# Performance work log

Hardware: AMD Instinct MI355X
Metric: run time of the kernel (lower is better)

## Reference

```python
import jax, jax.numpy as jnp
import numpy as np

B, L, INP, HID = 32, 1024, 600, 200

def setup_inputs() -> dict:
    key = jax.random.key(0)
    k1, k2, k3, k4 = jax.random.split(key, 4)
    return {
        "s1": jax.random.normal(k1, (B, L, INP), dtype=jnp.float32),
        "s2": jax.random.normal(k2, (B, L, INP), dtype=jnp.float32),
        "mask1": jnp.ones((B, L), dtype=jnp.float32),
        "mask2": jnp.ones((B, L), dtype=jnp.float32),
        "W1": jax.random.normal(k3, (INP, HID), dtype=jnp.float32) * (1.0 / np.sqrt(INP)),
        "b1": jnp.zeros((HID,), dtype=jnp.float32),
        "W2": jax.random.normal(k4, (HID, HID), dtype=jnp.float32) * (1.0 / np.sqrt(HID)),
        "b2": jnp.zeros((HID,), dtype=jnp.float32),
    }

def _mlp(x, W1, b1, W2, b2):
    # Dropout is identity at inference; two Linear+ReLU layers.
    h = jax.nn.relu(x @ W1 + b1)
    return jax.nn.relu(h @ W2 + b2)

def reference(s1, s2, mask1, mask2, W1, b1, W2, b2):
    h1 = _mlp(s1, W1, b1, W2, b2)          # (b, L, hid)
    h2 = _mlp(s2, W1, b1, W2, b2)          # (b, L, hid)
    e = jnp.einsum('bld,bmd->blm', h1, h2) # (b, LA, LB)
    # alpha: mask rows by mask1, softmax over LA (axis=1)
    e_alpha = jax.nn.softmax(e * mask1[:, :, None], axis=1)
    # beta: mask cols by mask2, softmax over LB (axis=2)
    e_beta = jax.nn.softmax(e * mask2[:, None, :], axis=2)
    alphas = jnp.einsum('blm,bld->bmd', e_alpha, s1) * mask2[:, :, None]
    betas = jnp.einsum('blm,bmd->bld', e_beta, s2) * mask1[:, :, None]
    return alphas, betas
```

## Files before the change

### kernel.cpp

```cpp
#include <hip/hip_runtime.h>
#include <math.h>

namespace {

constexpr int BB  = 32;
constexpr int LL  = 1024;
constexpr int INP = 600;
constexpr int HID = 200;
constexpr int RS  = BB * LL;
constexpr int DPAD = 640;

constexpr int BM = 128, BN = 128, KT = 8;

typedef __attribute__((ext_vector_type(8))) short short8v;
typedef __attribute__((ext_vector_type(8))) unsigned short ushort8v;
typedef __attribute__((ext_vector_type(4))) float f32x4;

__device__ __forceinline__ float relu(float x) { return fmaxf(x, 0.f); }

__device__ __forceinline__ unsigned short f2bf(float x) {
  union { float f; unsigned int u; } v; v.f = x;
  unsigned int r = v.u + 0x7FFFu + ((v.u >> 16) & 1u);
  return (unsigned short)(r >> 16);
}
__device__ __forceinline__ float bf2f(unsigned short h) {
  union { unsigned int u; float f; } v; v.u = ((unsigned int)h) << 16;
  return v.f;
}

__device__ __forceinline__ void gload16(const void* g, void* l) {
  __builtin_amdgcn_global_load_lds((const __attribute__((address_space(1))) void*)g,
                                   (__attribute__((address_space(3))) void*)l, 16, 0, 0);
}

__global__ __launch_bounds__(256) void wt_prep(
    const float* __restrict__ W, unsigned short* __restrict__ Whi, unsigned short* __restrict__ Wlo,
    int K, int KP)
{
  const int k = blockIdx.x * 256 + threadIdx.x;
  const int n = blockIdx.y;
  if (k >= KP) return;
  float v = (k < K && n < HID) ? W[(size_t)k * HID + n] : 0.f;
  unsigned short hi = f2bf(v);
  unsigned short lo = f2bf(v - bf2f(hi));
  Whi[(size_t)n * KP + k] = hi;
  Wlo[(size_t)n * KP + k] = lo;
}

template <bool MLP>
__global__ __launch_bounds__(256) void splitmm(
    const float* __restrict__ A0, const float* __restrict__ A1, long aZ, int lda, int ka,
    const float* __restrict__ Bf, long bZ,
    const unsigned short* __restrict__ Bhi, const unsigned short* __restrict__ Blo,
    int ldb, int kb, int ksteps,
    const float* __restrict__ bias,
    float* __restrict__ Out, int ldo, long oZ)
{
  __shared__ int4 sA[2048];
  __shared__ int4 sB[2048];
  const int z = blockIdx.z;
  const int m0 = blockIdx.x * 128, n0 = blockIdx.y * 128;
  const int tid = threadIdx.x, lane = tid & 63, w = tid >> 6;
  const int wr = w >> 1, wc = w & 1, fr = lane & 15, kg = lane >> 4;

  const float* __restrict__ A = MLP ? (z ? A1 : A0) : (A0 + (size_t)z * aZ);
  const float* __restrict__ Bp = MLP ? (const float*)nullptr : (Bf + (size_t)z * bZ);

  const int ar = tid >> 1, aseg = tid & 1;

  f32x4 acc[4][4];
#pragma unroll
  for (int mi = 0; mi < 4; ++mi)
#pragma unroll
    for (int ni = 0; ni < 4; ++ni) acc[mi][ni] = (f32x4){0.f, 0.f, 0.f, 0.f};

  for (int ks = 0; ks < ksteps; ++ks) {
    const int k0 = ks * 64;
    __syncthreads();
#pragma unroll
    for (int u = 0; u < 4; ++u) {
      const int c = aseg * 4 + u;
      const int gk = k0 + c * 8;
      float4 v0 = make_float4(0.f, 0.f, 0.f, 0.f), v1 = v0;
      if (gk < ka) {
        const float* p = A + (size_t)(m0 + ar) * lda + gk;
        v0 = *(const float4*)p;
        v1 = *(const float4*)(p + 4);
      }
      ushort8v hv, lv;
      hv[0] = f2bf(v0.x); lv[0] = f2bf(v0.x - bf2f(hv[0]));
      hv[1] = f2bf(v0.y); lv[1] = f2bf(v0.y - bf2f(hv[1]));
      hv[2] = f2bf(v0.z); lv[2] = f2bf(v0.z - bf2f(hv[2]));
      hv[3] = f2bf(v0.w); lv[3] = f2bf(v0.w - bf2f(hv[3]));
      hv[4] = f2bf(v1.x); lv[4] = f2bf(v1.x - bf2f(hv[4]));
      hv[5] = f2bf(v1.y); lv[5] = f2bf(v1.y - bf2f(hv[5]));
      hv[6] = f2bf(v1.z); lv[6] = f2bf(v1.z - bf2f(hv[6]));
      hv[7] = f2bf(v1.w); lv[7] = f2bf(v1.w - bf2f(hv[7]));
      const int slot = ar * 8 + (c ^ (ar & 7));
      *(ushort8v*)&sA[slot] = hv;
      *(ushort8v*)&sA[1024 + slot] = lv;
    }
    if (MLP) {
#pragma unroll
      for (int i = 0; i < 8; ++i) {
        const int s = w * 512 + i * 64 + lane;
        const int tens = s >> 10, rem = s & 1023, r = rem >> 3, kc = rem & 7;
        const int gc = kc ^ (r & 7);
        const unsigned short* src = (tens ? Blo : Bhi) + (size_t)(n0 + r) * ldb + k0 + gc * 8;
        gload16(src, (char*)sB + ((size_t)(w * 512 + i * 64)) * 16);
      }
    } else {
#pragma unroll
      for (int u = 0; u < 4; ++u) {
        const int c = aseg * 4 + u;
        const int gk = k0 + c * 8;
        float4 v0 = make_float4(0.f, 0.f, 0.f, 0.f), v1 = v0;
        if (gk < kb) {
          const float* p = Bp + (size_t)(n0 + ar) * ldb + gk;
          v0 = *(const float4*)p;
          v1 = *(const float4*)(p + 4);
        }
        ushort8v hv, lv;
        hv[0] = f2bf(v0.x); lv[0] = f2bf(v0.x - bf2f(hv[0]));
        hv[1] = f2bf(v0.y); lv[1] = f2bf(v0.y - bf2f(hv[1]));
        hv[2] = f2bf(v0.z); lv[2] = f2bf(v0.z - bf2f(hv[2]));
        hv[3] = f2bf(v0.w); lv[3] = f2bf(v0.w - bf2f(hv[3]));
        hv[4] = f2bf(v1.x); lv[4] = f2bf(v1.x - bf2f(hv[4]));
        hv[5] = f2bf(v1.y); lv[5] = f2bf(v1.y - bf2f(hv[5]));
        hv[6] = f2bf(v1.z); lv[6] = f2bf(v1.z - bf2f(hv[6]));
        hv[7] = f2bf(v1.w); lv[7] = f2bf(v1.w - bf2f(hv[7]));
        const int slot = ar * 8 + (c ^ (ar & 7));
        *(ushort8v*)&sB[slot] = hv;
        *(ushort8v*)&sB[1024 + slot] = lv;
      }
    }
    __syncthreads();
#pragma unroll
    for (int kk = 0; kk < 2; ++kk) {
      short8v ah[4], al[4], bh[4], bl[4];
#pragma unroll
      for (int mi = 0; mi < 4; ++mi) {
        const int row = wr * 64 + mi * 16 + fr;
        const int idx = row * 8 + ((kk * 4 + kg) ^ (row & 7));
        ah[mi] = *(const short8v*)&sA[idx];
        al[mi] = *(const short8v*)&sA[1024 + idx];
      }
#pragma unroll
      for (int ni = 0; ni < 4; ++ni) {
        const int row = wc * 64 + ni * 16 + fr;
        const int idx = row * 8 + ((kk * 4 + kg) ^ (row & 7));
        bh[ni] = *(const short8v*)&sB[idx];
        bl[ni] = *(const short8v*)&sB[1024 + idx];
      }
#pragma unroll
      for (int mi = 0; mi < 4; ++mi)
#pragma unroll
        for (int ni = 0; ni < 4; ++ni) {
          acc[mi][ni] = __builtin_amdgcn_mfma_f32_16x16x32_bf16(ah[mi], bh[ni], acc[mi][ni], 0, 0, 0);
          acc[mi][ni] = __builtin_amdgcn_mfma_f32_16x16x32_bf16(ah[mi], bl[ni], acc[mi][ni], 0, 0, 0);
          acc[mi][ni] = __builtin_amdgcn_mfma_f32_16x16x32_bf16(al[mi], bh[ni], acc[mi][ni], 0, 0, 0);
        }
    }
  }
#pragma unroll
  for (int ni = 0; ni < 4; ++ni) {
    const int gn = n0 + wc * 64 + ni * 16 + fr;
    if (!MLP || gn < HID) {
      const float bs = MLP ? bias[gn] : 0.f;
#pragma unroll
      for (int mi = 0; mi < 4; ++mi) {
#pragma unroll
        for (int r = 0; r < 4; ++r) {
          const int gm = m0 + wr * 64 + mi * 16 + kg * 4 + r;
          float v = acc[mi][ni][r] + bs;
          if (MLP) v = relu(v);
          Out[(size_t)z * oZ + (size_t)gm * ldo + gn] = v;
        }
      }
    }
  }
}

__global__ __launch_bounds__(256) void row_stats_pbeta(
    const float* __restrict__ E, const float* __restrict__ mask2,
    unsigned short* __restrict__ Pb)
{
  const int wid = threadIdx.x >> 6, lane = threadIdx.x & 63;
  const int r = blockIdx.x * 4 + wid;
  const int b = r >> 10;
  const float* __restrict__ row = E + (size_t)r * LL;
  const float* __restrict__ m2 = mask2 + b * LL;
  float v[16];
  float mx = -INFINITY;
#pragma unroll
  for (int i = 0; i < 4; ++i) {
    const int m = lane * 4 + i * 256;
    float4 e4 = *(const float4*)(row + m);
    float4 k4 = *(const float4*)(m2 + m);
    v[i * 4 + 0] = e4.x * k4.x; v[i * 4 + 1] = e4.y * k4.y;
    v[i * 4 + 2] = e4.z * k4.z; v[i * 4 + 3] = e4.w * k4.w;
    mx = fmaxf(mx, fmaxf(fmaxf(v[i * 4], v[i * 4 + 1]), fmaxf(v[i * 4 + 2], v[i * 4 + 3])));
  }
#pragma unroll
  for (int off = 32; off; off >>= 1) mx = fmaxf(mx, __shfl_xor(mx, off));
  float s = 0.f;
#pragma unroll
  for (int i = 0; i < 16; ++i) s += __expf(v[i] - mx);
#pragma unroll
  for (int off = 32; off; off >>= 1) s += __shfl_xor(s, off);
  const float ri = 1.f / s;
#pragma unroll
  for (int i = 0; i < 4; ++i) {
    const int m = lane * 4 + i * 256;
    ushort4 o;
    o.x = f2bf(__expf(v[i * 4 + 0] - mx) * ri);
    o.y = f2bf(__expf(v[i * 4 + 1] - mx) * ri);
    o.z = f2bf(__expf(v[i * 4 + 2] - mx) * ri);
    o.w = f2bf(__expf(v[i * 4 + 3] - mx) * ri);
    *(ushort4*)(Pb + (size_t)r * LL + m) = o;
  }
}

__global__ __launch_bounds__(256) void col_stats_p1(
    const float* __restrict__ E, const float* __restrict__ mask1,
    float* __restrict__ pmax, float* __restrict__ psum)
{
  const int b = blockIdx.z, lc = blockIdx.y;
  const int m = blockIdx.x * 256 + threadIdx.x;
  const float* __restrict__ e = E + (size_t)b * LL * LL;
  const float* __restrict__ m1 = mask1 + b * LL;
  float mx = -INFINITY, s = 0.f;
#pragma unroll 4
  for (int l = lc * 256; l < lc * 256 + 256; ++l) {
    const float v = e[(size_t)l * LL + m] * m1[l];
    if (v > mx) { s = s * __expf(mx - v) + 1.f; mx = v; }
    else        { s += __expf(v - mx); }
  }
  const int idx = (b * 4 + lc) * LL + m;
  pmax[idx] = mx; psum[idx] = s;
}

__global__ __launch_bounds__(256) void col_stats_p2(
    const float* __restrict__ pmax, const float* __restrict__ psum,
    float* __restrict__ cmax, float* __restrict__ cinv)
{
  const int b = blockIdx.y;
  const int m = blockIdx.x * 256 + threadIdx.x;
  float M = -INFINITY;
#pragma unroll
  for (int i = 0; i < 4; ++i) M = fmaxf(M, pmax[(b * 4 + i) * LL + m]);
  float S = 0.f;
#pragma unroll
  for (int i = 0; i < 4; ++i) S += psum[(b * 4 + i) * LL + m] * __expf(pmax[(b * 4 + i) * LL + m] - M);
  cmax[(size_t)b * LL + m] = M;
  cinv[(size_t)b * LL + m] = 1.f / S;
}

__global__ __launch_bounds__(256) void palpha_kernel(
    const float* __restrict__ E, const float* __restrict__ mask1,
    const float* __restrict__ cmax, const float* __restrict__ cinv,
    unsigned short* __restrict__ Pa)
{
  __shared__ float T[64][65];
  const int b = blockIdx.z;
  const int l0 = blockIdx.y * 64, m0 = blockIdx.x * 64;
  const int tid = threadIdx.x;
  const int rr = tid >> 4, c4 = (tid & 15) * 4;
  const float4 cm = *(const float4*)(cmax + b * LL + m0 + c4);
  const float4 ci = *(const float4*)(cinv + b * LL + m0 + c4);
#pragma unroll
  for (int it = 0; it < 4; ++it) {
    const int lloc = rr + it * 16;
    const int l = l0 + lloc;
    const float mk = mask1[b * LL + l];
    const float4 ev = *(const float4*)(E + ((size_t)b * LL + l) * LL + m0 + c4);
    T[c4 + 0][lloc] = __expf(ev.x * mk - cm.x) * ci.x;
    T[c4 + 1][lloc] = __expf(ev.y * mk - cm.y) * ci.y;
    T[c4 + 2][lloc] = __expf(ev.z * mk - cm.z) * ci.z;
    T[c4 + 3][lloc] = __expf(ev.w * mk - cm.w) * ci.w;
  }
  __syncthreads();
#pragma unroll
  for (int it = 0; it < 4; ++it) {
    const int mloc = rr + it * 16;
    ushort4 o;
    o.x = f2bf(T[mloc][c4 + 0]);
    o.y = f2bf(T[mloc][c4 + 1]);
    o.z = f2bf(T[mloc][c4 + 2]);
    o.w = f2bf(T[mloc][c4 + 3]);
    *(ushort4*)(Pa + ((size_t)b * LL + m0 + mloc) * LL + l0 + c4) = o;
  }
}

__global__ __launch_bounds__(256) void s_transpose(
    const float* __restrict__ S, unsigned short* __restrict__ St)
{
  __shared__ float T[64][65];
  const int b = blockIdx.z;
  const int l0 = blockIdx.y * 64, d0 = blockIdx.x * 64;
  const int tid = threadIdx.x;
  const int rr = tid >> 4, c4 = (tid & 15) * 4;
#pragma unroll
  for (int it = 0; it < 4; ++it) {
    const int lloc = rr + it * 16;
    const int l = l0 + lloc;
    float4 v = make_float4(0.f, 0.f, 0.f, 0.f);
    if (d0 + c4 < INP) v = *(const float4*)(S + ((size_t)b * LL + l) * INP + d0 + c4);
    T[c4 + 0][lloc] = v.x; T[c4 + 1][lloc] = v.y;
    T[c4 + 2][lloc] = v.z; T[c4 + 3][lloc] = v.w;
  }
  __syncthreads();
#pragma unroll
  for (int it = 0; it < 4; ++it) {
    const int dloc = rr + it * 16;
    ushort4 o;
    o.x = f2bf(T[dloc][c4 + 0]);
    o.y = f2bf(T[dloc][c4 + 1]);
    o.z = f2bf(T[dloc][c4 + 2]);
    o.w = f2bf(T[dloc][c4 + 3]);
    *(ushort4*)(St + ((size_t)b * DPAD + d0 + dloc) * LL + l0 + c4) = o;
  }
}

__global__ __launch_bounds__(256) void attn_gemm_bf16(
    const unsigned short* __restrict__ Ap, const unsigned short* __restrict__ Bt,
    const float* __restrict__ scale, float* __restrict__ Out)
{
  __shared__ int4 sAB[2048];
  __shared__ float s_sc[128];
  const int b  = blockIdx.z;
  const int n0 = blockIdx.x * 128;
  const int m0 = blockIdx.y * 128;
  const int tid = threadIdx.x;
  const int lane = tid & 63;
  const int w = tid >> 6;
  const int wr = w >> 1, wc = w & 1;
  const int fr = lane & 15, kg = lane >> 4;

  const unsigned short* __restrict__ A  = Ap + (size_t)b * LL * LL;
  const unsigned short* __restrict__ Bp = Bt + (size_t)b * DPAD * LL;

  if (tid < 128) s_sc[tid] = scale[b * LL + m0 + tid];

  f32x4 acc[4][4];
#pragma unroll
  for (int mi = 0; mi < 4; ++mi)
#pragma unroll
    for (int ni = 0; ni < 4; ++ni)
      acc[mi][ni] = (f32x4){0.f, 0.f, 0.f, 0.f};

  for (int k0 = 0; k0 < LL; k0 += 64) {
    __syncthreads();
#pragma unroll
    for (int i = 0; i < 8; ++i) {
      const int s = w * 512 + i * 64 + lane;
      const int tens = s >> 10, rem = s & 1023, r = rem >> 3, kc = rem & 7;
      const int gc = kc ^ (r & 7);
      const unsigned short* src = tens ? (Bp + (size_t)(n0 + r) * LL + k0 + gc * 8)
                                       : (A  + (size_t)(m0 + r) * LL + k0 + gc * 8);
      gload16(src, (char*)sAB + ((size_t)(w * 512 + i * 64)) * 16);
    }
    __syncthreads();
#pragma unroll
    for (int kk = 0; kk < 2; ++kk) {
      short8v a[4], bf[4];
#pragma unroll
      for (int mi = 0; mi < 4; ++mi) {
        const int row = wr * 64 + mi * 16 + fr;
        a[mi] = *(const short8v*)&sAB[row * 8 + ((kk * 4 + kg) ^ (row & 7))];
      }
#pragma unroll
      for (int ni = 0; ni < 4; ++ni) {
        const int row = wc * 64 + ni * 16 + fr;
        bf[ni] = *(const short8v*)&sAB[1024 + row * 8 + ((kk * 4 + kg) ^ (row & 7))];
      }
#pragma unroll
      for (int mi = 0; mi < 4; ++mi)
#pragma unroll
        for (int ni = 0; ni < 4; ++ni)
          acc[mi][ni] = __builtin_amdgcn_mfma_f32_16x16x32_bf16(a[mi], bf[ni], acc[mi][ni], 0, 0, 0);
    }
  }

#pragma unroll
  for (int mi = 0; mi < 4; ++mi) {
#pragma unroll
    for (int ni = 0; ni < 4; ++ni) {
      const int col = n0 + wc * 64 + ni * 16 + fr;
      if (col < INP) {
#pragma unroll
        for (int r = 0; r < 4; ++r) {
          const int mrow = wr * 64 + mi * 16 + kg * 4 + r;
          Out[((size_t)b * LL + m0 + mrow) * INP + col] = acc[mi][ni][r] * s_sc[mrow];
        }
      }
    }
  }
}

__device__ __forceinline__ void micro_8x8(const float (&sA)[KT][BM], const float (&sB)[KT][BN],
                                          float (&acc)[8][8], int tx, int ty)
{
#pragma unroll
  for (int kk = 0; kk < KT; ++kk) {
    float4 a0 = *(const float4*)&sA[kk][ty * 8];
    float4 a1 = *(const float4*)&sA[kk][ty * 8 + 4];
    float4 b0 = *(const float4*)&sB[kk][tx * 8];
    float4 b1 = *(const float4*)&sB[kk][tx * 8 + 4];
    float ar[8] = {a0.x, a0.y, a0.z, a0.w, a1.x, a1.y, a1.z, a1.w};
    float br[8] = {b0.x, b0.y, b0.z, b0.w, b1.x, b1.y, b1.z, b1.w};
#pragma unroll
    for (int i = 0; i < 8; ++i)
#pragma unroll
      for (int j = 0; j < 8; ++j)
        acc[i][j] = fmaf(ar[i], br[j], acc[i][j]);
  }
}

__global__ __launch_bounds__(256) void mlp_gemm(
    const float* __restrict__ A0, const float* __restrict__ A1,
    const float* __restrict__ W,  const float* __restrict__ bias,
    float* __restrict__ Out, int K)
{
  __shared__ __align__(16) float sA[KT][BM];
  __shared__ __align__(16) float sB[KT][BN];
  const int z = blockIdx.z;
  const float* __restrict__ A = z ? A1 : A0;
  float* __restrict__ out = Out + (size_t)z * RS * HID;
  const int m0 = blockIdx.x * BM;
  const int n0 = blockIdx.y * BN;
  const int tid = threadIdx.x;
  const int tx = tid & 15, ty = tid >> 4;
  const int am = tid & 127, akg = (tid >> 7) * 4;
  const int bn = (tid & 31) * 4, bkk = tid >> 5;

  float acc[8][8] = {};
  for (int k0 = 0; k0 < K; k0 += KT) {
    float4 av = *(const float4*)(A + (size_t)(m0 + am) * K + k0 + akg);
    sA[akg + 0][am] = av.x; sA[akg + 1][am] = av.y;
    sA[akg + 2][am] = av.z; sA[akg + 3][am] = av.w;
    const int gn = n0 + bn;
    float4 bv = make_float4(0.f, 0.f, 0.f, 0.f);
    if (gn < HID) bv = *(const float4*)(W + (size_t)(k0 + bkk) * HID + gn);
    *(float4*)&sB[bkk][bn] = bv;
    __syncthreads();
    micro_8x8(sA, sB, acc, tx, ty);
    __syncthreads();
  }
#pragma unroll
  for (int i = 0; i < 8; ++i) {
    const int m = m0 + ty * 8 + i;
#pragma unroll
    for (int j4 = 0; j4 < 8; j4 += 4) {
      const int n = n0 + tx * 8 + j4;
      if (n < HID) {
        float4 v;
        v.x = relu(acc[i][j4 + 0] + bias[n + 0]);
        v.y = relu(acc[i][j4 + 1] + bias[n + 1]);
        v.z = relu(acc[i][j4 + 2] + bias[n + 2]);
        v.w = relu(acc[i][j4 + 3] + bias[n + 3]);
        *(float4*)(out + (size_t)m * HID + n) = v;
      }
    }
  }
}

__global__ __launch_bounds__(256) void e_gemm(
    const float* __restrict__ H1, const float* __restrict__ H2, float* __restrict__ E)
{
  __shared__ __align__(16) float sA[KT][BM];
  __shared__ __align__(16) float sB[KT][BN];
  const int b = blockIdx.z;
  const float* __restrict__ A  = H1 + (size_t)b * LL * HID;
  const float* __restrict__ Bp = H2 + (size_t)b * LL * HID;
  float* __restrict__ e = E + (size_t)b * LL * LL;
  const int l0 = blockIdx.x * BM;
  const int m0 = blockIdx.y * BN;
  const int tid = threadIdx.x;
  const int tx = tid & 15, ty = tid >> 4;
  const int rr = tid & 127, kg = (tid >> 7) * 4;

  float acc[8][8] = {};
  for (int k0 = 0; k0 < HID; k0 += KT) {
    float4 av = *(const float4*)(A + (size_t)(l0 + rr) * HID + k0 + kg);
    sA[kg + 0][rr] = av.x; sA[kg + 1][rr] = av.y;
    sA[kg + 2][rr] = av.z; sA[kg + 3][rr] = av.w;
    float4 bv = *(const float4*)(Bp + (size_t)(m0 + rr) * HID + k0 + kg);
    sB[kg + 0][rr] = bv.x; sB[kg + 1][rr] = bv.y;
    sB[kg + 2][rr] = bv.z; sB[kg + 3][rr] = bv.w;
    __syncthreads();
    micro_8x8(sA, sB, acc, tx, ty);
    __syncthreads();
  }
#pragma unroll
  for (int i = 0; i < 8; ++i) {
    float* erow = e + (size_t)(l0 + ty * 8 + i) * LL + m0 + tx * 8;
    *(float4*)(erow)     = make_float4(acc[i][0], acc[i][1], acc[i][2], acc[i][3]);
    *(float4*)(erow + 4) = make_float4(acc[i][4], acc[i][5], acc[i][6], acc[i][7]);
  }
}

__global__ __launch_bounds__(256) void row_stats(
    const float* __restrict__ E, const float* __restrict__ mask2,
    float* __restrict__ rmax, float* __restrict__ rinv)
{
  const int wid = threadIdx.x >> 6, lane = threadIdx.x & 63;
  const int r = blockIdx.x * 4 + wid;
  const int b = r >> 10;
  const float* __restrict__ row = E + (size_t)r * LL;
  const float* __restrict__ m2 = mask2 + b * LL;
  float v[16];
  float mx = -INFINITY;
#pragma unroll
  for (int i = 0; i < 4; ++i) {
    const int m = lane * 4 + i * 256;
    float4 e4 = *(const float4*)(row + m);
    float4 k4 = *(const float4*)(m2 + m);
    v[i * 4 + 0] = e4.x * k4.x; v[i * 4 + 1] = e4.y * k4.y;
    v[i * 4 + 2] = e4.z * k4.z; v[i * 4 + 3] = e4.w * k4.w;
    mx = fmaxf(mx, fmaxf(fmaxf(v[i * 4], v[i * 4 + 1]), fmaxf(v[i * 4 + 2], v[i * 4 + 3])));
  }
#pragma unroll
  for (int off = 32; off; off >>= 1) mx = fmaxf(mx, __shfl_xor(mx, off));
  float s = 0.f;
#pragma unroll
  for (int i = 0; i < 16; ++i) s += __expf(v[i] - mx);
#pragma unroll
  for (int off = 32; off; off >>= 1) s += __shfl_xor(s, off);
  if (lane == 0) { rmax[r] = mx; rinv[r] = 1.f / s; }
}

__global__ __launch_bounds__(256) void alphas_gemm(
    const float* __restrict__ E, const float* __restrict__ S1,
    const float* __restrict__ mask1, const float* __restrict__ mask2,
    const float* __restrict__ cmax, const float* __restrict__ cinv,
    float* __restrict__ OutA)
{
  __shared__ __align__(16) float sA[KT][BM];
  __shared__ __align__(16) float sB[KT][BN];
  __shared__ __align__(16) float s_cm[BM], s_ci[BM], s_m2[BM];
  const int b = blockIdx.z;
  const float* __restrict__ e  = E  + (size_t)b * LL * LL;
  const float* __restrict__ s1 = S1 + (size_t)b * LL * INP;
  const int m0 = blockIdx.x * BM;
  const int d0 = blockIdx.y * BN;
  const int tid = threadIdx.x;
  const int tx = tid & 15, ty = tid >> 4;
  if (tid < BM) {
    s_cm[tid] = cmax[b * LL + m0 + tid];
    s_ci[tid] = cinv[b * LL + m0 + tid];
    s_m2[tid] = mask2[b * LL + m0 + tid];
  }
  __syncthreads();
  const int cc = (tid & 31) * 4, kk_ = tid >> 5;

  float acc[8][8] = {};
  for (int k0 = 0; k0 < LL; k0 += KT) {
    const int l = k0 + kk_;
    const float mk = mask1[b * LL + l];
    float4 ev = *(const float4*)(e + (size_t)l * LL + m0 + cc);
    float4 av;
    av.x = __expf(ev.x * mk - s_cm[cc + 0]) * s_ci[cc + 0];
    av.y = __expf(ev.y * mk - s_cm[cc + 1]) * s_ci[cc + 1];
    av.z = __expf(ev.z * mk - s_cm[cc + 2]) * s_ci[cc + 2];
    av.w = __expf(ev.w * mk - s_cm[cc + 3]) * s_ci[cc + 3];
    *(float4*)&sA[kk_][cc] = av;
    const int gd = d0 + cc;
    float4 bv = make_float4(0.f, 0.f, 0.f, 0.f);
    if (gd < INP) bv = *(const float4*)(s1 + (size_t)l * INP + gd);
    *(float4*)&sB[kk_][cc] = bv;
    __syncthreads();
    micro_8x8(sA, sB, acc, tx, ty);
    __syncthreads();
  }
#pragma unroll
  for (int i = 0; i < 8; ++i) {
    const int m = m0 + ty * 8 + i;
    const float mm = s_m2[ty * 8 + i];
    float* orow = OutA + ((size_t)b * LL + m) * INP;
#pragma unroll
    for (int j4 = 0; j4 < 8; j4 += 4) {
      const int d = d0 + tx * 8 + j4;
      if (d < INP) {
        *(float4*)(orow + d) = make_float4(acc[i][j4] * mm, acc[i][j4 + 1] * mm,
                                           acc[i][j4 + 2] * mm, acc[i][j4 + 3] * mm);
      }
    }
  }
}

__global__ __launch_bounds__(256) void betas_gemm(
    const float* __restrict__ E, const float* __restrict__ S2,
    const float* __restrict__ mask1, const float* __restrict__ mask2,
    const float* __restrict__ rmax, const float* __restrict__ rinv,
    float* __restrict__ OutB)
{
  __shared__ __align__(16) float sA[KT][BM];
  __shared__ __align__(16) float sB[KT][BN];
  __shared__ __align__(16) float s_rm[BM], s_ri[BM], s_m1[BM];
  const int b = blockIdx.z;
  const float* __restrict__ e  = E  + (size_t)b * LL * LL;
  const float* __restrict__ s2 = S2 + (size_t)b * LL * INP;
  const int l0 = blockIdx.x * BM;
  const int d0 = blockIdx.y * BN;
  const int tid = threadIdx.x;
  const int tx = tid & 15, ty = tid >> 4;
  if (tid < BM) {
    s_rm[tid] = rmax[b * LL + l0 + tid];
    s_ri[tid] = rinv[b * LL + l0 + tid];
    s_m1[tid] = mask1[b * LL + l0 + tid];
  }
  __syncthreads();
  const int al = tid & 127, akg = (tid >> 7) * 4;
  const int cc = (tid & 31) * 4, kk_ = tid >> 5;

  float acc[8][8] = {};
  for (int k0 = 0; k0 < LL; k0 += KT) {
    float4 ev = *(const float4*)(e + (size_t)(l0 + al) * LL + k0 + akg);
    float4 mk = *(const float4*)(mask2 + b * LL + k0 + akg);
    const float rm = s_rm[al], ri = s_ri[al];
    sA[akg + 0][al] = __expf(ev.x * mk.x - rm) * ri;
    sA[akg + 1][al] = __expf(ev.y * mk.y - rm) * ri;
    sA[akg + 2][al] = __expf(ev.z * mk.z - rm) * ri;
    sA[akg + 3][al] = __expf(ev.w * mk.w - rm) * ri;
    const int gd = d0 + cc;
    float4 bv = make_float4(0.f, 0.f, 0.f, 0.f);
    if (gd < INP) bv = *(const float4*)(s2 + (size_t)(k0 + kk_) * INP + gd);
    *(float4*)&sB[kk_][cc] = bv;
    __syncthreads();
    micro_8x8(sA, sB, acc, tx, ty);
    __syncthreads();
  }
#pragma unroll
  for (int i = 0; i < 8; ++i) {
    const int l = l0 + ty * 8 + i;
    const float mm = s_m1[ty * 8 + i];
    float* orow = OutB + ((size_t)b * LL + l) * INP;
#pragma unroll
    for (int j4 = 0; j4 < 8; j4 += 4) {
      const int d = d0 + tx * 8 + j4;
      if (d < INP) {
        *(float4*)(orow + d) = make_float4(acc[i][j4] * mm, acc[i][j4 + 1] * mm,
                                           acc[i][j4 + 2] * mm, acc[i][j4 + 3] * mm);
      }
    }
  }
}

}

extern "C" void kernel_launch(void* const* d_in, const int* in_sizes, int n_in,
                              void* d_out, int out_size, void* d_ws, size_t ws_size,
                              hipStream_t stream)
{
  const float* s1    = (const float*)d_in[0];
  const float* s2    = (const float*)d_in[1];
  const float* mask1 = (const float*)d_in[2];
  const float* mask2 = (const float*)d_in[3];
  const float* W1    = (const float*)d_in[4];
  const float* b1    = (const float*)d_in[5];
  const float* W2    = (const float*)d_in[6];
  const float* b2    = (const float*)d_in[7];

  char* ws = (char*)d_ws;
  float* outA = (float*)d_out;
  float* outB = outA + (size_t)BB * LL * INP;

  const size_t off_h  = 52428800;
  const size_t off_E  = 104857600;
  const size_t off_Pb = 239075328;
  const size_t TOTAL  = 306184192;

  if (ws_size >= TOTAL) {
    float* hmid = (float*)(ws + 0);
    float* h    = (float*)(ws + off_h);
    float* E    = (float*)(ws + off_E);
    unsigned short* Wt1hi = (unsigned short*)(ws + off_E);
    unsigned short* Wt1lo = Wt1hi + (size_t)256 * 640;
    unsigned short* Wt2hi = Wt1lo + (size_t)256 * 640;
    unsigned short* Wt2lo = Wt2hi + (size_t)256 * 256;
    unsigned short* Pb = (unsigned short*)(ws + off_Pb);
    unsigned short* Pa = (unsigned short*)(ws + 0);
    float* stats = (float*)(ws + 67108864);
    float* cmax = stats;
    float* cinv = cmax + RS;
    float* pmax = cinv + RS;
    float* psum = pmax + (size_t)BB * 4 * LL;
    unsigned short* s1t = (unsigned short*)(ws + off_E);
    unsigned short* s2t = s1t + (size_t)BB * DPAD * LL;

    wt_prep<<<dim3(3, 256), 256, 0, stream>>>(W1, Wt1hi, Wt1lo, INP, 640);
    wt_prep<<<dim3(1, 256), 256, 0, stream>>>(W2, Wt2hi, Wt2lo, HID, 256);
    splitmm<true><<<dim3(RS / 128, 2, 2), 256, 0, stream>>>(
        s1, s2, 0, INP, INP, nullptr, 0, Wt1hi, Wt1lo, 640, 0, 10,
        b1, hmid, HID, (long)RS * HID);
    splitmm<true><<<dim3(RS / 128, 2, 2), 256, 0, stream>>>(
        hmid, hmid + (size_t)RS * HID, 0, HID, HID, nullptr, 0, Wt2hi, Wt2lo, 256, 0, 4,
        b2, h, HID, (long)RS * HID);
    splitmm<false><<<dim3(8, 8, BB), 256, 0, stream>>>(
        h, nullptr, (long)LL * HID, HID, HID,
        h + (size_t)RS * HID, (long)LL * HID, nullptr, nullptr, HID, HID, 4,
        nullptr, E, LL, (long)LL * LL);
    row_stats_pbeta<<<dim3(RS / 4), 256, 0, stream>>>(E, mask2, Pb);
    col_stats_p1<<<dim3(4, 4, BB), 256, 0, stream>>>(E, mask1, pmax, psum);
    col_stats_p2<<<dim3(4, BB), 256, 0, stream>>>(pmax, psum, cmax, cinv);
    palpha_kernel<<<dim3(16, 16, BB), 256, 0, stream>>>(E, mask1, cmax, cinv, Pa);
    s_transpose<<<dim3(10, 16, BB), 256, 0, stream>>>(s1, s1t);
    s_transpose<<<dim3(10, 16, BB), 256, 0, stream>>>(s2, s2t);
    attn_gemm_bf16<<<dim3(5, 8, BB), 256, 0, stream>>>(Pb, s2t, mask1, outB);
    attn_gemm_bf16<<<dim3(5, 8, BB), 256, 0, stream>>>(Pa, s1t, mask2, outA);
  } else {
    float* h    = (float*)ws;
    float* hmid = h + (size_t)2 * RS * HID;
    float* E    = hmid;
    float* stats = hmid + (size_t)BB * LL * LL;
    float* rmax = stats;
    float* rinv = rmax + RS;
    float* cmax = rinv + RS;
    float* cinv = cmax + RS;
    float* pmax = cinv + RS;
    float* psum = pmax + (size_t)BB * 4 * LL;

    mlp_gemm<<<dim3(RS / BM, 2, 2), 256, 0, stream>>>(s1, s2, W1, b1, hmid, INP);
    mlp_gemm<<<dim3(RS / BM, 2, 2), 256, 0, stream>>>(hmid, hmid + (size_t)RS * HID, W2, b2, h, HID);
    e_gemm<<<dim3(LL / BM, LL / BN, BB), 256, 0, stream>>>(h, h + (size_t)RS * HID, E);
    row_stats<<<dim3(RS / 4), 256, 0, stream>>>(E, mask2, rmax, rinv);
    col_stats_p1<<<dim3(4, 4, BB), 256, 0, stream>>>(E, mask1, pmax, psum);
    col_stats_p2<<<dim3(4, BB), 256, 0, stream>>>(pmax, psum, cmax, cinv);
    alphas_gemm<<<dim3(LL / BM, (INP + BN - 1) / BN, BB), 256, 0, stream>>>(
        E, s1, mask1, mask2, cmax, cinv, outA);
    betas_gemm<<<dim3(LL / BM, (INP + BN - 1) / BN, BB), 256, 0, stream>>>(
        E, s2, mask1, mask2, rmax, rinv, outB);
  }

  (void)in_sizes; (void)n_in; (void)out_size;
}
```

Baseline: 926.4 us.

## Pre-split inputs to bf16 hi/lo and load all GEMM operands via LDS DMA

Adds a presplit kernel that converts s1/s2 into padded bf16 hi/lo arrays once, and makes the MLP GEMMs emit bf16 hi/lo split outputs directly. The unified splitmm2 kernel then loads both A and B operands with global_load_lds DMA instead of fp32 loads plus in-register conversion. This removes repeated fp32-to-bf16 splitting for every N tile and the VGPR and ALU pressure in the load path. In exchange it adds an extra pass over the inputs, writes split intermediates (the same total bytes as fp32), and reworks the workspace layout.

Result: no change. 927.7 us (+0.1%).

```diff
diff --git a/kernel.cpp b/kernel.cpp
--- a/kernel.cpp
+++ b/kernel.cpp
@@ -9,11 +9,12 @@
 constexpr int HID = 200;
 constexpr int RS  = BB * LL;
 constexpr int DPAD = 640;
+constexpr int KP1 = 640;
+constexpr int KP2 = 256;
 
 constexpr int BM = 128, BN = 128, KT = 8;
 
 typedef __attribute__((ext_vector_type(8))) short short8v;
-typedef __attribute__((ext_vector_type(8))) unsigned short ushort8v;
 typedef __attribute__((ext_vector_type(4))) float f32x4;
 
 __device__ __forceinline__ float relu(float x) { return fmaxf(x, 0.f); }
@@ -31,6 +32,26 @@
 __device__ __forceinline__ void gload16(const void* g, void* l) {
   __builtin_amdgcn_global_load_lds((const __attribute__((address_space(1))) void*)g,
                                    (__attribute__((address_space(3))) void*)l, 16, 0, 0);
+}
+
+__global__ __launch_bounds__(256) void presplit(
+    const float* __restrict__ S1, const float* __restrict__ S2,
+    unsigned short* __restrict__ Hi, unsigned short* __restrict__ Lo)
+{
+  const long idx = (long)blockIdx.x * 256 + threadIdx.x;
+  const long row = idx / 160;
+  const int  c4  = (int)(idx - row * 160) * 4;
+  const float* __restrict__ src = (row < RS) ? (S1 + row * (size_t)INP)
+                                             : (S2 + (row - RS) * (size_t)INP);
+  float4 v = make_float4(0.f, 0.f, 0.f, 0.f);
+  if (c4 < INP) v = *(const float4*)(src + c4);
+  ushort4 h4, l4;
+  h4.x = f2bf(v.x); l4.x = f2bf(v.x - bf2f(h4.x));
+  h4.y = f2bf(v.y); l4.y = f2bf(v.y - bf2f(h4.y));
+  h4.z = f2bf(v.z); l4.z = f2bf(v.z - bf2f(h4.z));
+  h4.w = f2bf(v.w); l4.w = f2bf(v.w - bf2f(h4.w));
+  *(ushort4*)(Hi + row * (size_t)KP1 + c4) = h4;
+  *(ushort4*)(Lo + row * (size_t)KP1 + c4) = l4;
 }
 
 __global__ __launch_bounds__(256) void wt_prep(
@@ -47,26 +68,29 @@
   Wlo[(size_t)n * KP + k] = lo;
 }
 
-template <bool MLP>
-__global__ __launch_bounds__(256) void splitmm(
-    const float* __restrict__ A0, const float* __restrict__ A1, long aZ, int lda, int ka,
-    const float* __restrict__ Bf, long bZ,
+template <bool SPLIT_OUT>
+__global__ __launch_bounds__(256) void splitmm2(
+    const unsigned short* __restrict__ Ahi, const unsigned short* __restrict__ Alo,
+    long aZ, int lda,
     const unsigned short* __restrict__ Bhi, const unsigned short* __restrict__ Blo,
-    int ldb, int kb, int ksteps,
-    const float* __restrict__ bias,
-    float* __restrict__ Out, int ldo, long oZ)
-{
-  __shared__ int4 sA[2048];
-  __shared__ int4 sB[2048];
+    long bZ, int ldb,
+    int ksteps, const float* __restrict__ bias,
+    unsigned short* __restrict__ OutHi, unsigned short* __restrict__ OutLo,
+    float* __restrict__ OutF, int ldo, long oZ)
+{
+  __shared__ int4 sL[4096];
   const int z = blockIdx.z;
   const int m0 = blockIdx.x * 128, n0 = blockIdx.y * 128;
   const int tid = threadIdx.x, lane = tid & 63, w = tid >> 6;
   const int wr = w >> 1, wc = w & 1, fr = lane & 15, kg = lane >> 4;
 
-  const float* __restrict__ A = MLP ? (z ? A1 : A0) : (A0 + (size_t)z * aZ);
-  const float* __restrict__ Bp = MLP ? (const float*)nullptr : (Bf + (size_t)z * bZ);
-
-  const int ar = tid >> 1, aseg = tid & 1;
+  const unsigned short* __restrict__ wbase =
+      (w == 0) ? (Ahi + (size_t)z * aZ) :
+      (w == 1) ? (Alo + (size_t)z * aZ) :
+      (w == 2) ? (Bhi + (size_t)z * bZ) :
+                 (Blo + (size_t)z * bZ);
+  const int wrow0 = (w < 2) ? m0 : n0;
+  const int wld   = (w < 2) ? lda : ldb;
 
   f32x4 acc[4][4];
 #pragma unroll
@@ -78,61 +102,12 @@
     const int k0 = ks * 64;
     __syncthreads();
 #pragma unroll
-    for (int u = 0; u < 4; ++u) {
-      const int c = aseg * 4 + u;
-      const int gk = k0 + c * 8;
-      float4 v0 = make_float4(0.f, 0.f, 0.f, 0.f), v1 = v0;
-      if (gk < ka) {
-        const float* p = A + (size_t)(m0 + ar) * lda + gk;
-        v0 = *(const float4*)p;
-        v1 = *(const float4*)(p + 4);
-      }
-      ushort8v hv, lv;
-      hv[0] = f2bf(v0.x); lv[0] = f2bf(v0.x - bf2f(hv[0]));
-      hv[1] = f2bf(v0.y); lv[1] = f2bf(v0.y - bf2f(hv[1]));
-      hv[2] = f2bf(v0.z); lv[2] = f2bf(v0.z - bf2f(hv[2]));
-      hv[3] = f2bf(v0.w); lv[3] = f2bf(v0.w - bf2f(hv[3]));
-      hv[4] = f2bf(v1.x); lv[4] = f2bf(v1.x - bf2f(hv[4]));
-      hv[5] = f2bf(v1.y); lv[5] = f2bf(v1.y - bf2f(hv[5]));
-      hv[6] = f2bf(v1.z); lv[6] = f2bf(v1.z - bf2f(hv[6]));
-      hv[7] = f2bf(v1.w); lv[7] = f2bf(v1.w - bf2f(hv[7]));
-      const int slot = ar * 8 + (c ^ (ar & 7));
-      *(ushort8v*)&sA[slot] = hv;
-      *(ushort8v*)&sA[1024 + slot] = lv;
-    }
-    if (MLP) {
-#pragma unroll
-      for (int i = 0; i < 8; ++i) {
-        const int s = w * 512 + i * 64 + lane;
-        const int tens = s >> 10, rem = s & 1023, r = rem >> 3, kc = rem & 7;
-        const int gc = kc ^ (r & 7);
-        const unsigned short* src = (tens ? Blo : Bhi) + (size_t)(n0 + r) * ldb + k0 + gc * 8;
-        gload16(src, (char*)sB + ((size_t)(w * 512 + i * 64)) * 16);
-      }
-    } else {
-#pragma unroll
-      for (int u = 0; u < 4; ++u) {
-        const int c = aseg * 4 + u;
-        const int gk = k0 + c * 8;
-        float4 v0 = make_float4(0.f, 0.f, 0.f, 0.f), v1 = v0;
-        if (gk < kb) {
-          const float* p = Bp + (size_t)(n0 + ar) * ldb + gk;
-          v0 = *(const float4*)p;
-          v1 = *(const float4*)(p + 4);
-        }
-        ushort8v hv, lv;
-        hv[0] = f2bf(v0.x); lv[0] = f2bf(v0.x - bf2f(hv[0]));
-        hv[1] = f2bf(v0.y); lv[1] = f2bf(v0.y - bf2f(hv[1]));
-        hv[2] = f2bf(v0.z); lv[2] = f2bf(v0.z - bf2f(hv[2]));
-        hv[3] = f2bf(v0.w); lv[3] = f2bf(v0.w - bf2f(hv[3]));
-        hv[4] = f2bf(v1.x); lv[4] = f2bf(v1.x - bf2f(hv[4]));
-        hv[5] = f2bf(v1.y); lv[5] = f2bf(v1.y - bf2f(hv[5]));
-        hv[6] = f2bf(v1.z); lv[6] = f2bf(v1.z - bf2f(hv[6]));
-        hv[7] = f2bf(v1.w); lv[7] = f2bf(v1.w - bf2f(hv[7]));
-        const int slot = ar * 8 + (c ^ (ar & 7));
-        *(ushort8v*)&sB[slot] = hv;
-        *(ushort8v*)&sB[1024 + slot] = lv;
-      }
+    for (int i = 0; i < 16; ++i) {
+      const int s = w * 1024 + i * 64 + lane;
+      const int rem = s & 1023, r = rem >> 3, kc = rem & 7;
+      const int gc = kc ^ (r & 7);
+      gload16(wbase + (size_t)(wrow0 + r) * wld + k0 + gc * 8,
+              (char*)sL + (size_t)s * 16);
     }
     __syncthreads();
 #pragma unroll
@@ -142,15 +117,15 @@
       for (int mi = 0; mi < 4; ++mi) {
         const int row = wr * 64 + mi * 16 + fr;
         const int idx = row * 8 + ((kk * 4 + kg) ^ (row & 7));
-        ah[mi] = *(const short8v*)&sA[idx];
-        al[mi] = *(const short8v*)&sA[1024 + idx];
+        ah[mi] = *(const short8v*)&sL[idx];
+        al[mi] = *(const short8v*)&sL[1024 + idx];
       }
 #pragma unroll
       for (int ni = 0; ni < 4; ++ni) {
         const int row = wc * 64 + ni * 16 + fr;
         const int idx = row * 8 + ((kk * 4 + kg) ^ (row & 7));
-        bh[ni] = *(const short8v*)&sB[idx];
-        bl[ni] = *(const short8v*)&sB[1024 + idx];
+        bh[ni] = *(const short8v*)&sL[2048 + idx];
+        bl[ni] = *(const short8v*)&sL[3072 + idx];
       }
 #pragma unroll
       for (int mi = 0; mi < 4; ++mi)
@@ -165,16 +140,31 @@
 #pragma unroll
   for (int ni = 0; ni < 4; ++ni) {
     const int gn = n0 + wc * 64 + ni * 16 + fr;
-    if (!MLP || gn < HID) {
-      const float bs = MLP ? bias[gn] : 0.f;
+    if (SPLIT_OUT) {
+      const bool valid = gn < HID;
+      const float bs = valid ? bias[gn] : 0.f;
 #pragma unroll
       for (int mi = 0; mi < 4; ++mi) {
 #pragma unroll
         for (int r = 0; r < 4; ++r) {
           const int gm = m0 + wr * 64 + mi * 16 + kg * 4 + r;
-          float v = acc[mi][ni][r] + bs;
-          if (MLP) v = relu(v);
-          Out[(size_t)z * oZ + (size_t)gm * ldo + gn] = v;
+          unsigned short hi = 0, lo = 0;
+          if (valid) {
+            float v = relu(acc[mi][ni][r] + bs);
+            hi = f2bf(v);
+            lo = f2bf(v - bf2f(hi));
+          }
+          OutHi[(size_t)z * oZ + (size_t)gm * ldo + gn] = hi;
+          OutLo[(size_t)z * oZ + (size_t)gm * ldo + gn] = lo;
+        }
+      }
+    } else {
+#pragma unroll
+      for (int mi = 0; mi < 4; ++mi) {
+#pragma unroll
+        for (int r = 0; r < 4; ++r) {
+          const int gm = m0 + wr * 64 + mi * 16 + kg * 4 + r;
+          OutF[(size_t)z * oZ + (size_t)gm * ldo + gn] = acc[mi][ni][r];
         }
       }
     }
@@ -666,19 +656,25 @@
   float* outA = (float*)d_out;
   float* outB = outA + (size_t)BB * LL * INP;
 
-  const size_t off_h  = 52428800;
-  const size_t off_E  = 104857600;
-  const size_t off_Pb = 239075328;
-  const size_t TOTAL  = 306184192;
+  const size_t off_splo = 83886080;
+  const size_t off_hmid = 167772160;
+  const size_t off_wt   = 234881024;
+  const size_t off_E    = 104857600;
+  const size_t off_Pb   = 239075328;
+  const size_t TOTAL    = 306184192;
 
   if (ws_size >= TOTAL) {
-    float* hmid = (float*)(ws + 0);
-    float* h    = (float*)(ws + off_h);
-    float* E    = (float*)(ws + off_E);
-    unsigned short* Wt1hi = (unsigned short*)(ws + off_E);
-    unsigned short* Wt1lo = Wt1hi + (size_t)256 * 640;
-    unsigned short* Wt2hi = Wt1lo + (size_t)256 * 640;
-    unsigned short* Wt2lo = Wt2hi + (size_t)256 * 256;
+    unsigned short* sp_hi = (unsigned short*)(ws + 0);
+    unsigned short* sp_lo = (unsigned short*)(ws + off_splo);
+    unsigned short* hmid_hi = (unsigned short*)(ws + off_hmid);
+    unsigned short* hmid_lo = hmid_hi + (size_t)2 * RS * KP2;
+    unsigned short* Wt1hi = (unsigned short*)(ws + off_wt);
+    unsigned short* Wt1lo = Wt1hi + (size_t)256 * KP1;
+    unsigned short* Wt2hi = Wt1lo + (size_t)256 * KP1;
+    unsigned short* Wt2lo = Wt2hi + (size_t)256 * KP2;
+    unsigned short* h_hi = (unsigned short*)(ws + 0);
+    unsigned short* h_lo = h_hi + (size_t)2 * RS * KP2;
+    float* E = (float*)(ws + off_E);
     unsigned short* Pb = (unsigned short*)(ws + off_Pb);
     unsigned short* Pa = (unsigned short*)(ws + 0);
     float* stats = (float*)(ws + 67108864);
@@ -689,18 +685,21 @@
     unsigned short* s1t = (unsigned short*)(ws + off_E);
     unsigned short* s2t = s1t + (size_t)BB * DPAD * LL;
 
-    wt_prep<<<dim3(3, 256), 256, 0, stream>>>(W1, Wt1hi, Wt1lo, INP, 640);
-    wt_prep<<<dim3(1, 256), 256, 0, stream>>>(W2, Wt2hi, Wt2lo, HID, 256);
-    splitmm<true><<<dim3(RS / 128, 2, 2), 256, 0, stream>>>(
-        s1, s2, 0, INP, INP, nullptr, 0, Wt1hi, Wt1lo, 640, 0, 10,
-        b1, hmid, HID, (long)RS * HID);
-    splitmm<true><<<dim3(RS / 128, 2, 2), 256, 0, stream>>>(
-        hmid, hmid + (size_t)RS * HID, 0, HID, HID, nullptr, 0, Wt2hi, Wt2lo, 256, 0, 4,
-        b2, h, HID, (long)RS * HID);
-    splitmm<false><<<dim3(8, 8, BB), 256, 0, stream>>>(
-        h, nullptr, (long)LL * HID, HID, HID,
-        h + (size_t)RS * HID, (long)LL * HID, nullptr, nullptr, HID, HID, 4,
-        nullptr, E, LL, (long)LL * LL);
+    wt_prep<<<dim3(3, 256), 256, 0, stream>>>(W1, Wt1hi, Wt1lo, INP, KP1);
+    wt_prep<<<dim3(1, 256), 256, 0, stream>>>(W2, Wt2hi, Wt2lo, HID, KP2);
+    presplit<<<dim3((2 * RS * 160) / 256), 256, 0, stream>>>(s1, s2, sp_hi, sp_lo);
+    splitmm2<true><<<dim3(RS / 128, 2, 2), 256, 0, stream>>>(
+        sp_hi, sp_lo, (long)RS * KP1, KP1,
+        Wt1hi, Wt1lo, 0, KP1, 10, b1,
+        hmid_hi, hmid_lo, nullptr, KP2, (long)RS * KP2);
+    splitmm2<true><<<dim3(RS / 128, 2, 2), 256, 0, stream>>>(
+        hmid_hi, hmid_lo, (long)RS * KP2, KP2,
+        Wt2hi, Wt2lo, 0, KP2, 4, b2,
+        h_hi, h_lo, nullptr, KP2, (long)RS * KP2);
+    splitmm2<false><<<dim3(8, 8, BB), 256, 0, stream>>>(
+        h_hi, h_lo, (long)LL * KP2, KP2,
+        h_hi + (size_t)RS * KP2, h_lo + (size_t)RS * KP2, (long)LL * KP2, KP2, 4, nullptr,
+        nullptr, nullptr, E, LL, (long)LL * LL);
     row_stats_pbeta<<<dim3(RS / 4), 256, 0, stream>>>(E, mask2, Pb);
     col_stats_p1<<<dim3(4, 4, BB), 256, 0, stream>>>(E, mask1, pmax, psum);
     col_stats_p2<<<dim3(4, BB), 256, 0, stream>>>(pmax, psum, cmax, cinv);
```
